# Kernel tuning notes

Measured on AMD Instinct MI355X. Metric: run time of the kernel, lower is better.

## Reference

```python
import jax, jax.numpy as jnp
import numpy as np

N, A, C, S = 65536, 1024, 1000, 2  # S = max aug multiplier from self.augs


def _update_cv(x, labels, cov_prior, ave_prior, amount_prior):
    # Efficient segment-reduce form of update_CV (original builds O(N*C*A) onehot tensor)
    cnt = jax.ops.segment_sum(jnp.ones((N,), x.dtype), labels, num_segments=C)  # [C]
    sum_c = jax.ops.segment_sum(x, labels, num_segments=C)                      # [C,A]
    cnt_c = jnp.where(cnt == 0, 1.0, cnt)                                       # Amount_CxA clamp
    ave = sum_c / cnt_c[:, None]                                                # ave_CxA
    var = jax.ops.segment_sum((x - ave[labels]) ** 2, labels, num_segments=C) / cnt_c[:, None]
    var = jnp.where(var == 0, 1e-10, var)
    w = (cnt / (cnt + amount_prior + 1e-10))[:, None]                           # weight_CV [C,1]
    additional = w * (1 - w) * (ave_prior - ave) ** 2
    new_cov = cov_prior * (1 - w) + var * w + additional
    new_ave = ave_prior * (1 - w) + ave * w
    new_amount = amount_prior + cnt
    return new_cov, new_ave, new_amount


def setup_inputs() -> dict:
    key = jax.random.key(0)
    ks = jax.random.split(key, 6)
    return {
        "x": jax.random.normal(ks[0], (N, A), jnp.float32),
        "eps": jax.random.normal(ks[1], (S, C, A), jnp.float32),
        "fc_w": jax.random.normal(ks[2], (C, A), jnp.float32) * 0.02,
        "fc_b": jnp.zeros((C,), jnp.float32),
        "ba_coeffi": jax.random.normal(ks[3], (C,), jnp.float32) * 0.1,
        "cov_prior": jax.random.uniform(ks[4], (C, A), jnp.float32) * 0.01,
        "ave_prior": jnp.zeros((C, A), jnp.float32),
        "amount_prior": jnp.zeros((C,), jnp.float32),
        "target_x": jax.random.randint(ks[5], (N,), 0, C).astype(jnp.int64),
    }


def reference(x, eps, fc_w, fc_b, ba_coeffi, cov_prior, ave_prior, amount_prior, target_x):
    # update_CV runs under torch.no_grad -> stop_gradient on stats
    new_cov, new_ave, _ = _update_cv(x, target_x, cov_prior, ave_prior, amount_prior)
    new_cov = jax.lax.stop_gradient(new_cov)
    new_ave = jax.lax.stop_gradient(new_ave)
    # Gaussian augmentation: Normal(loc=Ave, scale=CoVariance).sample((S,)) per class
    aug = new_ave[None, :, :] + new_cov[None, :, :] * eps  # [S,C,A]
    aug = aug.reshape(S * C, A)
    aug_labels = jnp.tile(jnp.arange(C, dtype=target_x.dtype), S)
    feats = jnp.concatenate([x, aug], axis=0)              # [N+S*C, A]
    labels_all = jnp.concatenate([target_x, aug_labels], axis=0)
    logits = feats @ fc_w.T + fc_b - ba_coeffi             # [N+S*C, C]
    logp = jax.nn.log_softmax(logits, axis=-1)
    loss = -jnp.mean(jnp.take_along_axis(logp, labels_all[:, None], axis=1))
    return loss
```

## Files before the change

kernel.cpp:

```cpp
#include <hip/hip_runtime.h>

#define NROWS 65536
#define ADIM  1024
#define CCLS  1000
#define SAUG  2
#define MROWS (NROWS + SAUG*CCLS)
#define MPAD  67584
#define NPAD  1024
#define NPART 4
#define NEG_INF (-3.0e38f)

typedef __bf16 bf16x8 __attribute__((ext_vector_type(8)));
typedef float  f32x4  __attribute__((ext_vector_type(4)));
typedef unsigned short u16;

__device__ __forceinline__ unsigned pk2bf(float a, float b){
  unsigned ua = __float_as_uint(a), ub = __float_as_uint(b);
  ua = (ua + 0x7FFFu + ((ua>>16)&1u)) >> 16;
  ub = (ub + 0x7FFFu + ((ub>>16)&1u)) >> 16;
  return ua | (ub<<16);
}
__device__ __forceinline__ float bflo(unsigned u){ return __uint_as_float((u & 0xFFFFu) << 16); }
__device__ __forceinline__ float bfhi(unsigned u){ return __uint_as_float(u & 0xFFFF0000u); }

__global__ void k_hist(const int* __restrict__ tgt, int* __restrict__ cnt){
  int i = blockIdx.x*blockDim.x + threadIdx.x;
  int stride = gridDim.x*blockDim.x;
  for (; i < NROWS; i += stride) atomicAdd(&cnt[tgt[i]], 1);
}

__global__ void k_scan(const int* __restrict__ cnt, int* __restrict__ start){
  __shared__ int s[1024];
  int t = threadIdx.x;
  int v = (t < CCLS) ? cnt[t] : 0;
  s[t] = v;
  __syncthreads();
  for (int off = 1; off < 1024; off <<= 1){
    int u = (t >= off) ? s[t-off] : 0;
    __syncthreads();
    s[t] += u;
    __syncthreads();
  }
  if (t < CCLS) start[t] = s[t] - v;
}

__global__ void k_scatter(const int* __restrict__ tgt, const int* __restrict__ start,
                          int* __restrict__ pos, int* __restrict__ sorted){
  int i = blockIdx.x*blockDim.x + threadIdx.x;
  int stride = gridDim.x*blockDim.x;
  for (; i < NROWS; i += stride){
    int c = tgt[i];
    int r = atomicAdd(&pos[c], 1);
    sorted[start[c] + r] = i;
  }
}

__global__ void k_cvt_x(const float* __restrict__ x, u16* __restrict__ xb){
  size_t i = ((size_t)blockIdx.x*blockDim.x + threadIdx.x)*8;
  float4 a = *(const float4*)(x+i);
  float4 b = *(const float4*)(x+i+4);
  uint4 o;
  o.x = pk2bf(a.x,a.y); o.y = pk2bf(a.z,a.w);
  o.z = pk2bf(b.x,b.y); o.w = pk2bf(b.z,b.w);
  *(uint4*)(xb+i) = o;
}

__global__ void k_pad(u16* __restrict__ xb){
  size_t i = ((size_t)blockIdx.x*blockDim.x + threadIdx.x)*8 + (size_t)MROWS*ADIM;
  uint4 z = {0u,0u,0u,0u};
  *(uint4*)(xb+i) = z;
}

__global__ void k_cvt_w(const float* __restrict__ w, u16* __restrict__ wb){
  size_t i = ((size_t)blockIdx.x*blockDim.x + threadIdx.x)*8;
  int row = (int)(i >> 10);
  uint4 o = {0u,0u,0u,0u};
  if (row < CCLS){
    float4 a = *(const float4*)(w+i);
    float4 b = *(const float4*)(w+i+4);
    o.x = pk2bf(a.x,a.y); o.y = pk2bf(a.z,a.w);
    o.z = pk2bf(b.x,b.y); o.w = pk2bf(b.z,b.w);
  }
  *(uint4*)(wb+i) = o;
}

__global__ void k_bias(const float* __restrict__ fc_b, const float* __restrict__ ba,
                       float* __restrict__ biasv){
  int c = blockIdx.x*blockDim.x + threadIdx.x;
  if (c < NPAD) biasv[c] = (c < CCLS) ? fc_b[c] - ba[c] : NEG_INF;
}

__global__ void k_stats(const u16* __restrict__ xb_in, const int* __restrict__ sorted,
                        const int* __restrict__ cnt, const int* __restrict__ start,
                        const float* __restrict__ amt_p, const float* __restrict__ cov_p,
                        const float* __restrict__ ave_p, const float* __restrict__ eps,
                        u16* __restrict__ xb){
  __shared__ int sidx[256];
  int c = blockIdx.x;
  int t = threadIdx.x;
  int col = t*4;
  int n = cnt[c];
  int st = start[c];
  float s[4] = {0.f,0.f,0.f,0.f}, q[4] = {0.f,0.f,0.f,0.f};
  for (int base = 0; base < n; base += 256){
    int m = min(256, n - base);
    __syncthreads();
    if (t < m) sidx[t] = sorted[st + base + t];
    __syncthreads();
    int i = 0;
    for (; i + 4 <= m; i += 4){
      int r0 = sidx[i], r1 = sidx[i+1], r2 = sidx[i+2], r3 = sidx[i+3];
      uint2 u0 = *(const uint2*)(xb_in + (size_t)r0*ADIM + col);
      uint2 u1 = *(const uint2*)(xb_in + (size_t)r1*ADIM + col);
      uint2 u2 = *(const uint2*)(xb_in + (size_t)r2*ADIM + col);
      uint2 u3 = *(const uint2*)(xb_in + (size_t)r3*ADIM + col);
      {
        float v0=bflo(u0.x), v1=bfhi(u0.x), v2=bflo(u0.y), v3=bfhi(u0.y);
        s[0]+=v0; s[1]+=v1; s[2]+=v2; s[3]+=v3;
        q[0]+=v0*v0; q[1]+=v1*v1; q[2]+=v2*v2; q[3]+=v3*v3;
      }
      {
        float v0=bflo(u1.x), v1=bfhi(u1.x), v2=bflo(u1.y), v3=bfhi(u1.y);
        s[0]+=v0; s[1]+=v1; s[2]+=v2; s[3]+=v3;
        q[0]+=v0*v0; q[1]+=v1*v1; q[2]+=v2*v2; q[3]+=v3*v3;
      }
      {
        float v0=bflo(u2.x), v1=bfhi(u2.x), v2=bflo(u2.y), v3=bfhi(u2.y);
        s[0]+=v0; s[1]+=v1; s[2]+=v2; s[3]+=v3;
        q[0]+=v0*v0; q[1]+=v1*v1; q[2]+=v2*v2; q[3]+=v3*v3;
      }
      {
        float v0=bflo(u3.x), v1=bfhi(u3.x), v2=bflo(u3.y), v3=bfhi(u3.y);
        s[0]+=v0; s[1]+=v1; s[2]+=v2; s[3]+=v3;
        q[0]+=v0*v0; q[1]+=v1*v1; q[2]+=v2*v2; q[3]+=v3*v3;
      }
    }
    for (; i < m; i++){
      int row = sidx[i];
      const uint2 uv = *(const uint2*)(xb_in + (size_t)row*ADIM + col);
      float v0 = bflo(uv.x), v1 = bfhi(uv.x), v2 = bflo(uv.y), v3 = bfhi(uv.y);
      s[0]+=v0; s[1]+=v1; s[2]+=v2; s[3]+=v3;
      q[0]+=v0*v0; q[1]+=v1*v1; q[2]+=v2*v2; q[3]+=v3*v3;
    }
  }
  float cf = (float)n;
  float cc = (n == 0) ? 1.f : cf;
  float wgt = cf / (cf + amt_p[c] + 1e-10f);
  float4 cv = *(const float4*)(cov_p + (size_t)c*ADIM + col);
  float4 av = *(const float4*)(ave_p + (size_t)c*ADIM + col);
  float cvp[4] = {cv.x,cv.y,cv.z,cv.w};
  float avp[4] = {av.x,av.y,av.z,av.w};
  float ncov[4], nave[4];
  #pragma unroll
  for (int j = 0; j < 4; j++){
    float ave = s[j]/cc;
    float var = (q[j] - 2.f*ave*s[j] + cf*ave*ave)/cc;
    if (var <= 0.f) var = 1e-10f;
    float add = wgt*(1.f-wgt)*(avp[j]-ave)*(avp[j]-ave);
    ncov[j] = cvp[j]*(1.f-wgt) + var*wgt + add;
    nave[j] = avp[j]*(1.f-wgt) + ave*wgt;
  }
  #pragma unroll
  for (int s_ = 0; s_ < SAUG; s_++){
    size_t eoff = ((size_t)(s_*CCLS + c))*ADIM + col;
    size_t roff = ((size_t)(NROWS + s_*CCLS + c))*ADIM + col;
    const float4 e = *(const float4*)(eps + eoff);
    uint2 o;
    o.x = pk2bf(nave[0]+ncov[0]*e.x, nave[1]+ncov[1]*e.y);
    o.y = pk2bf(nave[2]+ncov[2]*e.z, nave[3]+ncov[3]*e.w);
    *(uint2*)(xb + roff) = o;
  }
}

__global__ __launch_bounds__(512,2) void k_gemm_part(
    const u16* __restrict__ xb, const u16* __restrict__ wb,
    const float* __restrict__ biasv, const int* __restrict__ tgt,
    float* __restrict__ pm, float* __restrict__ pl, float* __restrict__ plab){
  extern __shared__ char smem[];
  const int t = threadIdx.x;
  const int lane = t & 63;
  const int wv = t >> 6;
  const int wr = wv >> 2;
  const int wc = wv & 3;
  const int col = lane & 15;
  const int quad = lane >> 4;

  const int bid = blockIdx.x;
  const int wg  = (bid & 7)*132 + (bid >> 3);
  const int sp  = wg & 3;
  const int row0 = (wg >> 2) * 256;

  const unsigned lds0 = (unsigned)(size_t)((__attribute__((address_space(3))) char*)smem);

  unsigned aB[4], bB[4];
  {
    unsigned linA = (unsigned)((wr*128 + col)*64 + quad*16);
    unsigned swzA = linA ^ (((linA >> 7) & 3u) << 4);
    unsigned linB = (unsigned)((wc*64 + col)*64 + quad*16);
    unsigned swzB = linB ^ (((linB >> 7) & 3u) << 4);
    #pragma unroll
    for (int qq = 0; qq < 4; qq++){
      aB[qq] = lds0 + qq*32768 + swzA;
      bB[qq] = lds0 + qq*32768 + 16384 + swzB;
    }
  }

  const u16* gA = xb + (size_t)row0*ADIM;
  const u16* gB = wb + (size_t)(sp*256)*ADIM;
  unsigned off_[2];
  const int ldsd = wv*1024;
  #pragma unroll
  for (int jj = 0; jj < 2; jj++){
    unsigned d = (unsigned)(jj*8192 + wv*1024 + lane*16);
    unsigned sv = d ^ (((d >> 7) & 3u) << 4);
    off_[jj] = (sv >> 6)*ADIM + ((sv & 63u) >> 1);
  }

#define STG4(TILE, NB) do{ \
  __builtin_amdgcn_global_load_lds((const __attribute__((address_space(1))) void*)(gA + off_[0] + (TILE)*32), \
      (__attribute__((address_space(3))) void*)(smem + (NB)*32768 + ldsd), 16, 0, 0); \
  __builtin_amdgcn_global_load_lds((const __attribute__((address_space(1))) void*)(gA + off_[1] + (TILE)*32), \
      (__attribute__((address_space(3))) void*)(smem + (NB)*32768 + 8192 + ldsd), 16, 0, 0); \
  __builtin_amdgcn_global_load_lds((const __attribute__((address_space(1))) void*)(gB + off_[0] + (TILE)*32), \
      (__attribute__((address_space(3))) void*)(smem + (NB)*32768 + 16384 + ldsd), 16, 0, 0); \
  __builtin_amdgcn_global_load_lds((const __attribute__((address_space(1))) void*)(gB + off_[1] + (TILE)*32), \
      (__attribute__((address_space(3))) void*)(smem + (NB)*32768 + 24576 + ldsd), 16, 0, 0); \
}while(0)

#define DSR(dst, base, off) asm volatile("ds_read_b128 %0, %1 offset:" #off : "=v"(dst) : "v"(base))
#define READT(QN, NA, NB) do{ \
  DSR(NA[0], aB[QN], 0);    DSR(NA[1], aB[QN], 1024); DSR(NA[2], aB[QN], 2048); DSR(NA[3], aB[QN], 3072); \
  DSR(NA[4], aB[QN], 4096); DSR(NA[5], aB[QN], 5120); DSR(NA[6], aB[QN], 6144); DSR(NA[7], aB[QN], 7168); \
  DSR(NB[0], bB[QN], 0);    DSR(NB[1], bB[QN], 1024); DSR(NB[2], bB[QN], 2048); DSR(NB[3], bB[QN], 3072); \
}while(0)

#define MFMAT(CA, CB) do{ \
  _Pragma("unroll") \
  for (int m_ = 0; m_ < 8; m_++){ \
    _Pragma("unroll") \
    for (int n_ = 0; n_ < 4; n_++) \
      acc[m_][n_] = __builtin_amdgcn_mfma_f32_16x16x32_bf16(CA[m_], CB[n_], acc[m_][n_], 0, 0, 0); \
  } \
}while(0)

#define BODY(TILE3, QN, QS, CA, CB, NA, NB) do{ \
  __builtin_amdgcn_s_barrier(); \
  __builtin_amdgcn_sched_barrier(0); \
  STG4((TILE3), QS); \
  asm volatile("s_waitcnt vmcnt(4)" ::: "memory"); \
  __builtin_amdgcn_sched_barrier(0); \
  READT(QN, NA, NB); \
  asm volatile("s_waitcnt lgkmcnt(12)" ::: "memory"); \
  __builtin_amdgcn_sched_barrier(0); \
  __builtin_amdgcn_s_setprio(1); \
  MFMAT(CA, CB); \
  __builtin_amdgcn_s_setprio(0); \
  __builtin_amdgcn_sched_barrier(0); \
}while(0)

  f32x4 acc[8][4];
  const f32x4 z = {0.f,0.f,0.f,0.f};
  #pragma unroll
  for (int m = 0; m < 8; m++)
    #pragma unroll
    for (int n = 0; n < 4; n++) acc[m][n] = z;

  bf16x8 pA[8], pB[4], oA[8], oB[4];

  STG4(0, 0); STG4(1, 1); STG4(2, 2);
  asm volatile("s_waitcnt vmcnt(4)" ::: "memory");
  __builtin_amdgcn_sched_barrier(0);
  __builtin_amdgcn_s_barrier();
  __builtin_amdgcn_sched_barrier(0);
  READT(0, pA, pB);

  for (int b4 = 0; b4 < 7; b4++){
    const int kt = b4*4;
    BODY(kt+3, 1, 3, pA, pB, oA, oB);
    BODY(kt+4, 2, 0, oA, oB, pA, pB);
    BODY(kt+5, 3, 1, pA, pB, oA, oB);
    BODY(kt+6, 0, 2, oA, oB, pA, pB);
  }

  BODY(31, 1, 3, pA, pB, oA, oB);
  __builtin_amdgcn_s_barrier();
  __builtin_amdgcn_sched_barrier(0);
  asm volatile("s_waitcnt vmcnt(0)" ::: "memory");
  __builtin_amdgcn_sched_barrier(0);
  READT(2, pA, pB);
  asm volatile("s_waitcnt lgkmcnt(12)" ::: "memory");
  __builtin_amdgcn_sched_barrier(0);
  __builtin_amdgcn_s_setprio(1);
  MFMAT(oA, oB);
  __builtin_amdgcn_s_setprio(0);
  __builtin_amdgcn_s_barrier();
  __builtin_amdgcn_sched_barrier(0);
  READT(3, oA, oB);
  asm volatile("s_waitcnt lgkmcnt(12)" ::: "memory");
  __builtin_amdgcn_sched_barrier(0);
  __builtin_amdgcn_s_setprio(1);
  MFMAT(pA, pB);
  __builtin_amdgcn_s_setprio(0);
  asm volatile("s_waitcnt lgkmcnt(0)" ::: "memory");
  __builtin_amdgcn_sched_barrier(0);
  __builtin_amdgcn_s_setprio(1);
  MFMAT(oA, oB);
  __builtin_amdgcn_s_setprio(0);

#undef BODY
#undef MFMAT
#undef READT
#undef DSR
#undef STG4

  float bias[4];
  #pragma unroll
  for (int n = 0; n < 4; n++) bias[n] = biasv[sp*256 + wc*64 + n*16 + col];

  __syncthreads();
  float* red = (float*)smem;

  #pragma unroll
  for (int m = 0; m < 8; m++){
    #pragma unroll
    for (int rg = 0; rg < 4; rg++){
      const int rb = wr*128 + m*16 + quad*4 + rg;
      const int gr = row0 + rb;
      int lbl = -1;
      if (gr < NROWS) lbl = tgt[gr];
      else if (gr < MROWS){ int a_ = gr - NROWS; lbl = (a_ < CCLS) ? a_ : a_ - CCLS; }
      float lg[4];
      float mx = NEG_INF, lv = NEG_INF;
      #pragma unroll
      for (int n = 0; n < 4; n++){
        float v = acc[m][n][rg] + bias[n];
        lg[n] = v;
        mx = fmaxf(mx, v);
        int c = sp*256 + wc*64 + n*16 + col;
        lv = (c == lbl) ? v : lv;
      }
      #pragma unroll
      for (int o = 1; o < 16; o <<= 1) mx = fmaxf(mx, __shfl_xor(mx, o));
      float se = 0.f;
      #pragma unroll
      for (int n = 0; n < 4; n++) se += __expf(lg[n] - mx);
      #pragma unroll
      for (int o = 1; o < 16; o <<= 1) se += __shfl_xor(se, o);
      #pragma unroll
      for (int o = 1; o < 16; o <<= 1) lv = fmaxf(lv, __shfl_xor(lv, o));
      if (col == 0){
        red[0*1024 + rb*4 + wc] = mx;
        red[1*1024 + rb*4 + wc] = se;
        red[2*1024 + rb*4 + wc] = lv;
      }
    }
  }
  __syncthreads();
  if (t < 256){
    float m0 = red[t*4+0], m1 = red[t*4+1], m2 = red[t*4+2], m3 = red[t*4+3];
    float mx = fmaxf(fmaxf(m0,m1), fmaxf(m2,m3));
    float l  = red[1024+t*4+0]*__expf(m0-mx) + red[1024+t*4+1]*__expf(m1-mx)
             + red[1024+t*4+2]*__expf(m2-mx) + red[1024+t*4+3]*__expf(m3-mx);
    float lv = fmaxf(fmaxf(red[2048+t*4+0],red[2048+t*4+1]),
                     fmaxf(red[2048+t*4+2],red[2048+t*4+3]));
    size_t idx = (size_t)sp*MPAD + (size_t)(row0 + t);
    pm[idx]   = mx;
    pl[idx]   = l;
    plab[idx] = lv;
  }
}

__global__ void k_merge(const float* __restrict__ pm, const float* __restrict__ pl,
                        const float* __restrict__ plab, float* __restrict__ out){
  int r = blockIdx.x*256 + threadIdx.x;
  float v = 0.f;
  if (r < MROWS){
    float m = NEG_INF, lb = NEG_INF;
    #pragma unroll
    for (int s = 0; s < NPART; s++){
      m  = fmaxf(m,  pm[(size_t)s*MPAD + r]);
      lb = fmaxf(lb, plab[(size_t)s*MPAD + r]);
    }
    float l = 0.f;
    #pragma unroll
    for (int s = 0; s < NPART; s++)
      l += pl[(size_t)s*MPAD + r]*__expf(pm[(size_t)s*MPAD + r] - m);
    v = (m + __logf(l) - lb) * (1.0f/(float)MROWS);
  }
  #pragma unroll
  for (int o = 32; o > 0; o >>= 1) v += __shfl_xor(v, o);
  if ((threadIdx.x & 63) == 0) atomicAdd(out, v);
}

extern "C" void kernel_launch(void* const* d_in, const int* in_sizes, int n_in,
                              void* d_out, int out_size, void* d_ws, size_t ws_size,
                              hipStream_t stream) {
  const float* x     = (const float*)d_in[0];
  const float* eps   = (const float*)d_in[1];
  const float* fc_w  = (const float*)d_in[2];
  const float* fc_b  = (const float*)d_in[3];
  const float* ba    = (const float*)d_in[4];
  const float* cov_p = (const float*)d_in[5];
  const float* ave_p = (const float*)d_in[6];
  const float* amt_p = (const float*)d_in[7];
  const int*   tgt   = (const int*)d_in[8];
  float* out = (float*)d_out;

  char* ws = (char*)d_ws;
  u16*   xb    = (u16*)(ws);
  u16*   wb    = (u16*)(ws + 138412032u);
  float* biasv = (float*)(ws + 140509184u);
  int*   sorted= (int*)(ws + 140513280u);
  int*   cnt   = (int*)(ws + 140775424u);
  int*   pos   = (int*)(ws + 140779520u);
  int*   start = (int*)(ws + 140783616u);
  float* pm    = (float*)(ws + 140787712u);
  float* pl    = (float*)(ws + 142950400u);
  float* plab  = (float*)(ws + 145113088u);

  static int cfg = 0;
  if (!cfg){
    hipFuncSetAttribute((const void*)k_gemm_part,
                        hipFuncAttributeMaxDynamicSharedMemorySize, 131072);
    cfg = 1;
  }

  hipMemsetAsync(cnt, 0, 12288, stream);
  hipMemsetAsync(out, 0, sizeof(float), stream);

  k_hist   <<<256, 256, 0, stream>>>(tgt, cnt);
  k_scan   <<<1, 1024, 0, stream>>>(cnt, start);
  k_scatter<<<256, 256, 0, stream>>>(tgt, start, pos, sorted);
  k_cvt_x  <<<32768, 256, 0, stream>>>(x, xb);
  k_pad    <<<24, 256, 0, stream>>>(xb);
  k_cvt_w  <<<512, 256, 0, stream>>>(fc_w, wb);
  k_bias   <<<4, 256, 0, stream>>>(fc_b, ba, biasv);
  k_stats  <<<CCLS, 256, 0, stream>>>(xb, sorted, cnt, start, amt_p, cov_p, ave_p, eps, xb);
  k_gemm_part<<<1056, 512, 131072, stream>>>(xb, wb, biasv, tgt, pm, pl, plab);
  k_merge  <<<264, 256, 0, stream>>>(pm, pl, plab, out);
}
```

Before: 719.2 us.

## Restructure GEMM main loop into fine-grained ping-pong LDS pipeline with fewer registers

Replaces the four-stage LDS ring with two 64-KB halves holding two K-subtiles each. Each step loads half of a sub-tile's A fragments plus B fragments into 8 register vectors, then issues 16 MFMAs between barriers, with global-to-LDS loads for later tiles interleaved. It also changes the LDS swizzle pattern and global addressing. The aim is to cut fragment register pressure and interleave loads with MFMAs more finely. The cost is many more barriers and full lgkmcnt(0) waits per step, which may serialize LDS reads with compute.

```diff
diff --git a/kernel.cpp b/kernel.cpp
--- a/kernel.cpp
+++ b/kernel.cpp
@@ -13,6 +13,9 @@
 typedef __bf16 bf16x8 __attribute__((ext_vector_type(8)));
 typedef float  f32x4  __attribute__((ext_vector_type(4)));
 typedef unsigned short u16;
+
+#define AS1 __attribute__((address_space(1)))
+#define AS3 __attribute__((address_space(3)))
 
 __device__ __forceinline__ unsigned pk2bf(float a, float b){
   unsigned ua = __float_as_uint(a), ub = __float_as_uint(b);
@@ -190,72 +193,55 @@
   const int sp  = wg & 3;
   const int row0 = (wg >> 2) * 256;
 
-  const unsigned lds0 = (unsigned)(size_t)((__attribute__((address_space(3))) char*)smem);
-
-  unsigned aB[4], bB[4];
-  {
-    unsigned linA = (unsigned)((wr*128 + col)*64 + quad*16);
-    unsigned swzA = linA ^ (((linA >> 7) & 3u) << 4);
-    unsigned linB = (unsigned)((wc*64 + col)*64 + quad*16);
-    unsigned swzB = linB ^ (((linB >> 7) & 3u) << 4);
-    #pragma unroll
-    for (int qq = 0; qq < 4; qq++){
-      aB[qq] = lds0 + qq*32768 + swzA;
-      bB[qq] = lds0 + qq*32768 + 16384 + swzB;
-    }
-  }
-
-  const u16* gA = xb + (size_t)row0*ADIM;
-  const u16* gB = wb + (size_t)(sp*256)*ADIM;
-  unsigned off_[2];
+  const unsigned lds0 = (unsigned)(size_t)((AS3 char*)smem);
+
+  const unsigned swzq = (unsigned)((quad*16) ^ (((lane>>3)&1)*32));
+  const unsigned vA0 = lds0 + (unsigned)((wr*128 + col)*64) + swzq;
+  const unsigned vB0 = lds0 + 32768u + (unsigned)((wc*64 + col)*64) + swzq;
+  const unsigned vA1 = vA0 + 65536u;
+  const unsigned vB1 = vB0 + 65536u;
+
   const int ldsd = wv*1024;
-  #pragma unroll
-  for (int jj = 0; jj < 2; jj++){
-    unsigned d = (unsigned)(jj*8192 + wv*1024 + lane*16);
-    unsigned sv = d ^ (((d >> 7) & 3u) << 4);
-    off_[jj] = (sv >> 6)*ADIM + ((sv & 63u) >> 1);
-  }
-
-#define STG4(TILE, NB) do{ \
-  __builtin_amdgcn_global_load_lds((const __attribute__((address_space(1))) void*)(gA + off_[0] + (TILE)*32), \
-      (__attribute__((address_space(3))) void*)(smem + (NB)*32768 + ldsd), 16, 0, 0); \
-  __builtin_amdgcn_global_load_lds((const __attribute__((address_space(1))) void*)(gA + off_[1] + (TILE)*32), \
-      (__attribute__((address_space(3))) void*)(smem + (NB)*32768 + 8192 + ldsd), 16, 0, 0); \
-  __builtin_amdgcn_global_load_lds((const __attribute__((address_space(1))) void*)(gB + off_[0] + (TILE)*32), \
-      (__attribute__((address_space(3))) void*)(smem + (NB)*32768 + 16384 + ldsd), 16, 0, 0); \
-  __builtin_amdgcn_global_load_lds((const __attribute__((address_space(1))) void*)(gB + off_[1] + (TILE)*32), \
-      (__attribute__((address_space(3))) void*)(smem + (NB)*32768 + 24576 + ldsd), 16, 0, 0); \
+  const int csw = ((lane&3)*8) ^ (((lane>>5)&1)*16);
+  const int rT  = wv*16 + (lane>>2);
+  const u16* pA = xb + (size_t)(row0 + rT)*ADIM + csw;
+  const u16* pB = wb + (size_t)(sp*256 + rT)*ADIM + csw;
+
+#define STG(PTR, DOFF, KOFF) do{ \
+  __builtin_amdgcn_global_load_lds((const AS1 void*)((PTR) + (KOFF)), \
+      (AS3 void*)(smem + (DOFF) + ldsd), 16, 0, 0); \
+  __builtin_amdgcn_global_load_lds((const AS1 void*)((PTR) + (KOFF) + 131072), \
+      (AS3 void*)(smem + (DOFF) + 8192 + ldsd), 16, 0, 0); \
 }while(0)
 
-#define DSR(dst, base, off) asm volatile("ds_read_b128 %0, %1 offset:" #off : "=v"(dst) : "v"(base))
-#define READT(QN, NA, NB) do{ \
-  DSR(NA[0], aB[QN], 0);    DSR(NA[1], aB[QN], 1024); DSR(NA[2], aB[QN], 2048); DSR(NA[3], aB[QN], 3072); \
-  DSR(NA[4], aB[QN], 4096); DSR(NA[5], aB[QN], 5120); DSR(NA[6], aB[QN], 6144); DSR(NA[7], aB[QN], 7168); \
-  DSR(NB[0], bB[QN], 0);    DSR(NB[1], bB[QN], 1024); DSR(NB[2], bB[QN], 2048); DSR(NB[3], bB[QN], 3072); \
+#define DSR(dst, base, OFF) asm volatile("ds_read_b128 %0, %1 offset:" #OFF : "=v"(dst) : "v"(base))
+#define RDA_K0LO(V) do{ DSR(a0,V,0);     DSR(a1,V,1024);  DSR(a2,V,2048);  DSR(a3,V,3072);  }while(0)
+#define RDA_K0HI(V) do{ DSR(a0,V,4096);  DSR(a1,V,5120);  DSR(a2,V,6144);  DSR(a3,V,7168);  }while(0)
+#define RDA_K1LO(V) do{ DSR(a0,V,16384); DSR(a1,V,17408); DSR(a2,V,18432); DSR(a3,V,19456); }while(0)
+#define RDA_K1HI(V) do{ DSR(a0,V,20480); DSR(a1,V,21504); DSR(a2,V,22528); DSR(a3,V,23552); }while(0)
+#define RDB_K0(V)   do{ DSR(b0,V,0);     DSR(b1,V,1024);  DSR(b2,V,2048);  DSR(b3,V,3072);  }while(0)
+#define RDB_K1(V)   do{ DSR(b0,V,16384); DSR(b1,V,17408); DSR(b2,V,18432); DSR(b3,V,19456); }while(0)
+
+#define MM(A_,B_,C_) C_ = __builtin_amdgcn_mfma_f32_16x16x32_bf16(A_,B_,C_,0,0,0)
+#define MF16(MS) do{ \
+  MM(a0,b0,acc[MS+0][0]); MM(a0,b1,acc[MS+0][1]); MM(a0,b2,acc[MS+0][2]); MM(a0,b3,acc[MS+0][3]); \
+  MM(a1,b0,acc[MS+1][0]); MM(a1,b1,acc[MS+1][1]); MM(a1,b2,acc[MS+1][2]); MM(a1,b3,acc[MS+1][3]); \
+  MM(a2,b0,acc[MS+2][0]); MM(a2,b1,acc[MS+2][1]); MM(a2,b2,acc[MS+2][2]); MM(a2,b3,acc[MS+2][3]); \
+  MM(a3,b0,acc[MS+3][0]); MM(a3,b1,acc[MS+3][1]); MM(a3,b2,acc[MS+3][2]); MM(a3,b3,acc[MS+3][3]); \
 }while(0)
 
-#define MFMAT(CA, CB) do{ \
-  _Pragma("unroll") \
-  for (int m_ = 0; m_ < 8; m_++){ \
-    _Pragma("unroll") \
-    for (int n_ = 0; n_ < 4; n_++) \
-      acc[m_][n_] = __builtin_amdgcn_mfma_f32_16x16x32_bf16(CA[m_], CB[n_], acc[m_][n_], 0, 0, 0); \
-  } \
-}while(0)
-
-#define BODY(TILE3, QN, QS, CA, CB, NA, NB) do{ \
+#define VMW4 asm volatile("s_waitcnt vmcnt(4)" ::: "memory")
+#define VMW0 asm volatile("s_waitcnt vmcnt(0)" ::: "memory")
+#define BARMF(MS) do{ \
+  __builtin_amdgcn_sched_barrier(0); \
   __builtin_amdgcn_s_barrier(); \
-  __builtin_amdgcn_sched_barrier(0); \
-  STG4((TILE3), QS); \
-  asm volatile("s_waitcnt vmcnt(4)" ::: "memory"); \
-  __builtin_amdgcn_sched_barrier(0); \
-  READT(QN, NA, NB); \
-  asm volatile("s_waitcnt lgkmcnt(12)" ::: "memory"); \
+  asm volatile("s_waitcnt lgkmcnt(0)" ::: "memory"); \
   __builtin_amdgcn_sched_barrier(0); \
   __builtin_amdgcn_s_setprio(1); \
-  MFMAT(CA, CB); \
+  MF16(MS); \
   __builtin_amdgcn_s_setprio(0); \
   __builtin_amdgcn_sched_barrier(0); \
+  __builtin_amdgcn_s_barrier(); \
 }while(0)
 
   f32x4 acc[8][4];
@@ -265,53 +251,50 @@
     #pragma unroll
     for (int n = 0; n < 4; n++) acc[m][n] = z;
 
-  bf16x8 pA[8], pB[4], oA[8], oB[4];
-
-  STG4(0, 0); STG4(1, 1); STG4(2, 2);
-  asm volatile("s_waitcnt vmcnt(4)" ::: "memory");
+  bf16x8 a0,a1,a2,a3,b0,b1,b2,b3;
+
+  STG(pA, 0,      0);  STG(pB, 32768,  0);
+  STG(pA, 16384,  32); STG(pB, 49152,  32);
+  STG(pA, 65536,  64); STG(pB, 98304,  64);
+  VMW0;
   __builtin_amdgcn_sched_barrier(0);
   __builtin_amdgcn_s_barrier();
-  __builtin_amdgcn_sched_barrier(0);
-  READT(0, pA, pB);
-
-  for (int b4 = 0; b4 < 7; b4++){
-    const int kt = b4*4;
-    BODY(kt+3, 1, 3, pA, pB, oA, oB);
-    BODY(kt+4, 2, 0, oA, oB, pA, pB);
-    BODY(kt+5, 3, 1, pA, pB, oA, oB);
-    BODY(kt+6, 0, 2, oA, oB, pA, pB);
-  }
-
-  BODY(31, 1, 3, pA, pB, oA, oB);
-  __builtin_amdgcn_s_barrier();
-  __builtin_amdgcn_sched_barrier(0);
-  asm volatile("s_waitcnt vmcnt(0)" ::: "memory");
-  __builtin_amdgcn_sched_barrier(0);
-  READT(2, pA, pB);
-  asm volatile("s_waitcnt lgkmcnt(12)" ::: "memory");
-  __builtin_amdgcn_sched_barrier(0);
-  __builtin_amdgcn_s_setprio(1);
-  MFMAT(oA, oB);
-  __builtin_amdgcn_s_setprio(0);
-  __builtin_amdgcn_s_barrier();
-  __builtin_amdgcn_sched_barrier(0);
-  READT(3, oA, oB);
-  asm volatile("s_waitcnt lgkmcnt(12)" ::: "memory");
-  __builtin_amdgcn_sched_barrier(0);
-  __builtin_amdgcn_s_setprio(1);
-  MFMAT(pA, pB);
-  __builtin_amdgcn_s_setprio(0);
-  asm volatile("s_waitcnt lgkmcnt(0)" ::: "memory");
-  __builtin_amdgcn_sched_barrier(0);
-  __builtin_amdgcn_s_setprio(1);
-  MFMAT(oA, oB);
-  __builtin_amdgcn_s_setprio(0);
-
-#undef BODY
-#undef MFMAT
-#undef READT
+
+  for (int it = 0; it < 7; it++){
+    const int kb = it*128;
+    RDA_K0LO(vA0); RDB_K0(vB0); STG(pA, 81920,  kb+96);  BARMF(0);
+    RDA_K0HI(vA0);              STG(pB, 114688, kb+96);  VMW4; BARMF(4);
+    RDA_K1LO(vA0); RDB_K1(vB0); STG(pA, 0,      kb+128); BARMF(0);
+    RDA_K1HI(vA0);              STG(pB, 32768,  kb+128); BARMF(4);
+    RDA_K0LO(vA1); RDB_K0(vB1); STG(pA, 16384,  kb+160); BARMF(0);
+    RDA_K0HI(vA1);              STG(pB, 49152,  kb+160); VMW4; BARMF(4);
+    RDA_K1LO(vA1); RDB_K1(vB1); STG(pA, 65536,  kb+192); BARMF(0);
+    RDA_K1HI(vA1);              STG(pB, 98304,  kb+192); BARMF(4);
+  }
+  {
+    RDA_K0LO(vA0); RDB_K0(vB0); STG(pA, 81920,  992);    BARMF(0);
+    RDA_K0HI(vA0);              STG(pB, 114688, 992);    VMW4; BARMF(4);
+    RDA_K1LO(vA0); RDB_K1(vB0);                          BARMF(0);
+    RDA_K1HI(vA0);                                       BARMF(4);
+    RDA_K0LO(vA1); RDB_K0(vB1);                          BARMF(0);
+    RDA_K0HI(vA1);                                       VMW0; BARMF(4);
+    RDA_K1LO(vA1); RDB_K1(vB1);                          BARMF(0);
+    RDA_K1HI(vA1);                                       BARMF(4);
+  }
+
+#undef BARMF
+#undef VMW0
+#undef VMW4
+#undef MF16
+#undef MM
+#undef RDB_K1
+#undef RDB_K0
+#undef RDA_K1HI
+#undef RDA_K1LO
+#undef RDA_K0HI
+#undef RDA_K0LO
 #undef DSR
-#undef STG4
+#undef STG
 
   float bias[4];
   #pragma unroll
```

Result: faster. 677.9 us (-5.7%).
